# Performance work log

Measured on AMD Instinct MI355X. Metric: run time of the kernel, lower is better.

Reference implementation:

```python
import jax, jax.numpy as jnp
import numpy as np

D = 1024          # d_model
N = 256           # d_state
SQN = 16          # sqrt(d_state), number of blocks / block size
LR = 0.1
BASE_DECAY = 0.05


def setup_inputs() -> dict:
    key = jax.random.key(0)
    ks = jax.random.split(key, 7)
    B, S = 8, 1024
    x = jax.random.normal(ks[0], (B, S, D), dtype=jnp.float32)
    Wk = jax.random.normal(ks[1], (N, D), dtype=jnp.float32) * 0.02
    Wv = jax.random.normal(ks[2], (N, D), dtype=jnp.float32) * 0.02
    Wg = jax.random.normal(ks[3], (1, D), dtype=jnp.float32) * 0.02
    bg = jnp.zeros((1,), dtype=jnp.float32)
    Wo = jax.random.normal(ks[4], (D, N), dtype=jnp.float32) * 0.02
    bo = jnp.zeros((D,), dtype=jnp.float32)
    return {"x": x, "Wk": Wk, "Wv": Wv, "Wg": Wg, "bg": bg, "Wo": Wo, "bo": bo}


def _forward(x, Wk, Wv, Wg, bg, Wo, bo):
    B, S, _ = x.shape
    n = SQN
    dtype = x.dtype
    K = (x @ Wk.T).reshape(B, S, n, n)
    V = (x @ Wv.T).reshape(B, S, n, n)
    gate = jax.nn.sigmoid(x @ Wg.T + bg)  # (B, S, 1)

    w_init = jnp.broadcast_to(jnp.eye(n, dtype=dtype), (n, n, n))       # block identity
    w0 = jnp.broadcast_to(w_init, (B, n, n, n)).astype(dtype)

    def step(carry, inp):
        w1, w2, strength, last_seen, t = carry
        kt, vt, gt = inp  # (B,n,n), (B,n,n), (B,1)
        t = t + 1.0
        # block-diagonal matmuls: hidden[b,i,:] = kt[b,i,:] @ w1[b,i]
        hidden = jnp.einsum('bij,bijk->bik', kt, w1)
        hr = jnp.swapaxes(hidden, -1, -2)  # monarch routing (transpose blocks)
        vt_pred = jnp.einsum('bij,bijk->bik', hr, w2)
        error = vt_pred - vt
        activity = jnp.linalg.norm(kt, axis=-1)  # (B,n)
        delta_t = t - last_seen
        time_gate = 1.0 / jnp.maximum(jnp.log1p(delta_t / 10.0), 1.0)
        decay_rate = BASE_DECAY / (1.0 + strength * time_gate)  # (B,n)
        # TTT gradient step on fast weights
        grad2 = jnp.einsum('bip,biq->bipq', hr, error)
        grad_h = jnp.einsum('bij,bikj->bik', error, w2)
        grad1 = jnp.einsum('bip,biq->bipq', kt, grad_h)
        step_lr = LR * gt[:, :, None, None]  # (B,1,1,1)
        w1 = w1 - step_lr * grad1
        w2 = w2 - step_lr * grad2
        # Ebbinghaus strength / spacing bookkeeping
        err_norm = jnp.linalg.norm(error.reshape(error.shape[0], -1), axis=-1)  # (B,)
        recon_quality = 1.0 / (1.0 + err_norm)
        spacing = jnp.log1p(delta_t) * activity  # (B,n)
        strength = strength + recon_quality[:, None] * spacing * gt * 0.05
        last_seen = jnp.where(activity > 0.1, t, last_seen)
        # decay toward identity init
        df = decay_rate[:, :, None, None]
        w1 = w1 * (1.0 - df) + w_init * df
        w2 = w2 * (1.0 - df) + w_init * df
        yt = jnp.swapaxes(vt_pred, -1, -2).reshape(vt_pred.shape[0], n * n)
        return (w1, w2, strength, last_seen, t), (yt, err_norm)

    carry0 = (w0, w0,
              jnp.zeros((B, n), dtype),
              jnp.zeros((B, n), dtype),
              jnp.asarray(0.0, dtype))
    xs = (jnp.swapaxes(K, 0, 1), jnp.swapaxes(V, 0, 1), jnp.swapaxes(gate, 0, 1))
    _, (ys, errs) = jax.lax.scan(step, carry0, xs)
    output = jnp.swapaxes(ys, 0, 1) @ Wo.T + bo       # (B,S,D)
    error_signal = jnp.swapaxes(errs, 0, 1)[..., None]  # (B,S,1)
    return output, error_signal


def reference(x, Wk, Wv, Wg, bg, Wo, bo):
    return _forward(x, Wk, Wv, Wg, bg, Wo, bo)
```

## Files before the change

kernel.cpp:

```cpp
#include <hip/hip_runtime.h>
#include <hip/hip_bf16.h>

#define B_DIM 8
#define S_DIM 1024
#define D_DIM 1024
#define N_DIM 256
#define M_ROWS (B_DIM * S_DIM)

typedef __attribute__((ext_vector_type(8))) short bf16x8;
typedef __attribute__((ext_vector_type(8))) unsigned short u16x8;
typedef __attribute__((ext_vector_type(4))) float f32x4;
typedef __attribute__((ext_vector_type(2))) float f32x2;

static __device__ __forceinline__ unsigned short f2bf(float f) {
  union { __hip_bfloat16 h; unsigned short s; } u;
  u.h = __float2bfloat16(f);
  return u.s;
}

static __device__ __forceinline__ float log1p_fast(float x) {
  return __logf(1.0f + x);
}

static __device__ __forceinline__ float hsum4(f32x4 v) {
  f32x2 lo = {v[0], v[1]}, hi = {v[2], v[3]};
  f32x2 t = lo + hi;
  return t[0] + t[1];
}

static __device__ __forceinline__ float dpp_swap1(float x) {
  int r = __builtin_amdgcn_update_dpp(0, __builtin_bit_cast(int, x),
                                      0xB1, 0xF, 0xF, true);
  return __builtin_bit_cast(float, r);
}
static __device__ __forceinline__ float pair_sum(float x) {
  return x + dpp_swap1(x);
}

#define LDS_BARRIER()                                         \
  do {                                                        \
    asm volatile("s_waitcnt lgkmcnt(0)" ::: "memory");        \
    __builtin_amdgcn_s_barrier();                             \
    asm volatile("" ::: "memory");                            \
  } while (0)

__global__ __launch_bounds__(256) void gemm_kv(const float* __restrict__ x,
                                               const float* __restrict__ Wk,
                                               const float* __restrict__ Wv,
                                               float* __restrict__ KV) {
  __shared__ unsigned short lsA[128 * 40];
  __shared__ unsigned short lsB[128 * 40];
  const int tid = threadIdx.x;
  const int row0 = blockIdx.y * 128;
  const int col0 = blockIdx.x * 128;
  const float* Bsrc = (col0 < 256) ? (Wk + (size_t)col0 * 1024)
                                   : (Wv + (size_t)(col0 - 256) * 1024);
  const int sr = tid >> 1, sh = tid & 1;
  const float* ap = x + (size_t)(row0 + sr) * 1024 + sh * 16;
  const float* bp = Bsrc + (size_t)sr * 1024 + sh * 16;
  unsigned short* wa = &lsA[sr * 40 + sh * 16];
  unsigned short* wb = &lsB[sr * 40 + sh * 16];

  const int lane = tid & 63;
  const int w = tid >> 6, wr = w >> 1, wc = w & 1;
  const int fr = lane & 15, fk = lane >> 4;

  f32x4 acc[4][4];
#pragma unroll
  for (int m = 0; m < 4; ++m)
#pragma unroll
    for (int n = 0; n < 4; ++n) acc[m][n] = (f32x4){0.f, 0.f, 0.f, 0.f};

  for (int kt = 0; kt < 32; ++kt) {
    const float* a = ap + kt * 32;
    const float* b = bp + kt * 32;
    f32x4 A0 = *(const f32x4*)(a + 0), A1 = *(const f32x4*)(a + 4);
    f32x4 A2 = *(const f32x4*)(a + 8), A3 = *(const f32x4*)(a + 12);
    f32x4 B0 = *(const f32x4*)(b + 0), B1 = *(const f32x4*)(b + 4);
    f32x4 B2 = *(const f32x4*)(b + 8), B3 = *(const f32x4*)(b + 12);
    u16x8 pa0, pa1, pb0, pb1;
#pragma unroll
    for (int e = 0; e < 4; ++e) {
      pa0[e] = f2bf(A0[e]); pa0[e + 4] = f2bf(A1[e]);
      pa1[e] = f2bf(A2[e]); pa1[e + 4] = f2bf(A3[e]);
      pb0[e] = f2bf(B0[e]); pb0[e + 4] = f2bf(B1[e]);
      pb1[e] = f2bf(B2[e]); pb1[e + 4] = f2bf(B3[e]);
    }
    *(u16x8*)wa = pa0; *(u16x8*)(wa + 8) = pa1;
    *(u16x8*)wb = pb0; *(u16x8*)(wb + 8) = pb1;
    __syncthreads();
    bf16x8 af[4], bfr[4];
#pragma unroll
    for (int m = 0; m < 4; ++m)
      af[m] = *(const bf16x8*)(&lsA[(wr * 64 + m * 16 + fr) * 40 + fk * 8]);
#pragma unroll
    for (int n = 0; n < 4; ++n)
      bfr[n] = *(const bf16x8*)(&lsB[(wc * 64 + n * 16 + fr) * 40 + fk * 8]);
#pragma unroll
    for (int m = 0; m < 4; ++m)
#pragma unroll
      for (int n = 0; n < 4; ++n)
        acc[m][n] = __builtin_amdgcn_mfma_f32_16x16x32_bf16(af[m], bfr[n],
                                                            acc[m][n], 0, 0, 0);
    __syncthreads();
  }
#pragma unroll
  for (int m = 0; m < 4; ++m)
#pragma unroll
    for (int n = 0; n < 4; ++n) {
      const int col = col0 + wc * 64 + n * 16 + fr;
#pragma unroll
      for (int r = 0; r < 4; ++r) {
        const int row = row0 + wr * 64 + m * 16 + fk * 4 + r;
        KV[(size_t)row * 512 + col] = acc[m][n][r];
      }
    }
}

__global__ __launch_bounds__(256) void gate_kernel(const float* __restrict__ x,
                                                   const float* __restrict__ Wg,
                                                   const float* __restrict__ bg,
                                                   float* __restrict__ gate) {
  const int row = blockIdx.x * 4 + (threadIdx.x >> 6);
  const int lane = threadIdx.x & 63;
  const f32x4* xr = (const f32x4*)(x + (size_t)row * 1024);
  const f32x4* wg = (const f32x4*)Wg;
  float s = 0.f;
#pragma unroll
  for (int c = 0; c < 4; ++c) {
    f32x4 a = xr[lane + 64 * c];
    f32x4 wv = wg[lane + 64 * c];
    s += a[0] * wv[0] + a[1] * wv[1] + a[2] * wv[2] + a[3] * wv[3];
  }
#pragma unroll
  for (int off = 32; off >= 1; off >>= 1) s += __shfl_xor(s, off, 64);
  if (lane == 0) gate[row] = 1.f / (1.f + __expf(-(s + bg[0])));
}

__global__ __launch_bounds__(256) void wo_perm(const float* __restrict__ Wo,
                                               float* __restrict__ WoP) {
  const int d = blockIdx.x;
  const int c = threadIdx.x;
  WoP[(size_t)d * 256 + c] = Wo[(size_t)d * 256 + ((c & 15) * 16 + (c >> 4))];
}

__global__ __launch_bounds__(256) void act_kernel(const float* __restrict__ KV,
                                                  float* __restrict__ actv) {
  const int idx = blockIdx.x * 256 + threadIdx.x;
  const int bs = idx >> 4, i = idx & 15;
  const f32x4* p = (const f32x4*)(KV + (size_t)bs * 512 + i * 16);
  f32x4 a0 = p[0], a1 = p[1], a2 = p[2], a3 = p[3];
  f32x4 s = a0 * a0 + a1 * a1 + a2 * a2 + a3 * a3;
  actv[idx] = sqrtf(hsum4(s));
}

__global__ __launch_bounds__(512) void scan_kernel(const float* __restrict__ KV,
                                                   const float* __restrict__ gate,
                                                   const float* __restrict__ actv,
                                                   unsigned short* __restrict__ ysbf,
                                                   float* __restrict__ err_out) {
  const int b = blockIdx.x;
  const int tid = threadIdx.x;
  const int i = tid >> 5;
  const int k = (tid >> 1) & 15;
  const int h = tid & 1;
  const int j0 = h * 8;

  __shared__ __align__(16) float hidT[2][16 * 20 + 4];
  __shared__ __align__(16) float errS[256];
  __shared__ __align__(16) float red[2][8];

  if (tid < 16) ((float*)red)[tid] = 0.f;

  f32x4 w1q[2], w2q[2], w2tq[2], eyeq[2];
#pragma unroll
  for (int r = 0; r < 2; ++r) {
    f32x4 v;
#pragma unroll
    for (int e = 0; e < 4; ++e) v[e] = ((j0 + 4 * r + e) == k) ? 1.f : 0.f;
    w1q[r] = v; w2q[r] = v; w2tq[r] = v; eyeq[r] = v;
  }
  float strength = 0.f, last_seen = 0.f, pend = 0.f;

  const float* Kb = KV + (size_t)b * S_DIM * 512;
  const float* Gb = gate + (size_t)b * S_DIM;
  const float* Ab = actv + (size_t)b * S_DIM * 16;
  float* Eb = err_out + (size_t)b * S_DIM;

  const int offK = i * 16 + j0;
  const int offV = 256 + i * 16 + k;

  f32x4 kqA0, kqA1, kqB0, kqB1;
  float vtA, vtB, gA, gB, aA, aB;
  {
    kqA0 = *(const f32x4*)(Kb + offK);
    kqA1 = *(const f32x4*)(Kb + offK + 4);
    vtA = Kb[offV]; gA = Gb[0]; aA = Ab[i];
    kqB0 = *(const f32x4*)(Kb + 512 + offK);
    kqB1 = *(const f32x4*)(Kb + 512 + offK + 4);
    vtB = Kb[512 + offV]; gB = Gb[1]; aB = Ab[16 + i];
  }

  const float* pPre = Kb + 1024;
  const float* pG = Gb + 2;
  const float* pA = Ab + 32 + i;
  unsigned short* pY = ysbf + (size_t)b * S_DIM * 256 + i * 16 + k;

  auto step = [&](int s, f32x4& kq0, f32x4& kq1, float& vt, float& gv,
                  float& av) {
    const int pb = s & 1;
    const float t = (float)(s + 1);

    f32x4 hacc = kq0 * w1q[0] + kq1 * w1q[1];
    const float hidden = pair_sum(hsum4(hacc));
    hidT[pb][k * 20 + i] = hidden;

    const float delta = t - last_seen;
    const float m_pre = fmaxf(log1p_fast(delta * 0.1f), 1.f);
    const float pend_new = log1p_fast(delta) * av * gv * 0.05f;
    const bool seen = (av > 0.1f);

    LDS_BARRIER();

    const f32x4 hq0 = *(const f32x4*)&hidT[pb][i * 20 + j0];
    const f32x4 hq1 = *(const f32x4*)&hidT[pb][i * 20 + j0 + 4];
    const float hkk = hidT[pb][i * 20 + k];

    {
      const f32x4* rp = (const f32x4*)&red[1 - pb][0];
      const f32x4 rs = rp[0] + rp[1];
      const float en = sqrtf(hsum4(rs));
      strength += pend * __builtin_amdgcn_rcpf(1.f + en);
      if (tid == 0 && s != 0) Eb[s - 1] = en;
    }
    const float df = 0.05f * m_pre * __builtin_amdgcn_rcpf(m_pre + strength);
    const float am = 1.f - df;

    f32x4 vacc = hq0 * w2q[0] + hq1 * w2q[1];
    const float vt_pred = pair_sum(hsum4(vacc));
    *pY = f2bf(vt_pred);

    const float err = vt_pred - vt;

    errS[i * 16 + k] = err;
    asm volatile("s_waitcnt lgkmcnt(0)" ::: "memory");
    const f32x4 eq0 = *(const f32x4*)&errS[i * 16 + j0];
    const f32x4 eq1 = *(const f32x4*)&errS[i * 16 + j0 + 4];

    const f32x4 eacc = eq0 * eq0 + eq1 * eq1;
    const float e2row = pair_sum(hsum4(eacc));
    const float e2pair = e2row + __shfl_xor(e2row, 32, 64);
    if ((tid & 63) == 0) red[pb][tid >> 6] = e2pair;

    const f32x4 gacc = eq0 * w2tq[0] + eq1 * w2tq[1];
    const float gh = pair_sum(hsum4(gacc));

    const float slr = 0.1f * gv;
    const float nsga = -slr * gh * am;
    const float nsea = -slr * err * am;
    const float nsha = -slr * hkk * am;
#pragma unroll
    for (int r = 0; r < 2; ++r) {
      const f32x4 kr = (r == 0) ? kq0 : kq1;
      const f32x4 hr = (r == 0) ? hq0 : hq1;
      const f32x4 er = (r == 0) ? eq0 : eq1;
      const f32x4 dfr = eyeq[r] * df;
      w1q[r] = w1q[r] * am + (kr * nsga + dfr);
      w2q[r] = w2q[r] * am + (hr * nsea + dfr);
      w2tq[r] = w2tq[r] * am + (er * nsha + dfr);
    }

    pend = pend_new;
    if (seen) last_seen = t;

    kq0 = *(const f32x4*)(pPre + offK);
    kq1 = *(const f32x4*)(pPre + offK + 4);
    vt = pPre[offV];
    gv = *pG;
    av = *pA;
    pPre += 512; pG += 1; pA += 16; pY += 256;
  };

  for (int s = 0; s < S_DIM; s += 2) {
    step(s, kqA0, kqA1, vtA, gA, aA);
    step(s + 1, kqB0, kqB1, vtB, gB, aB);
  }
  LDS_BARRIER();
  if (tid == 0) {
    const f32x4* rp = (const f32x4*)&red[1][0];
    const f32x4 rs = rp[0] + rp[1];
    Eb[S_DIM - 1] = sqrtf(hsum4(rs));
  }
}

__global__ __launch_bounds__(256) void gemm_out(const unsigned short* __restrict__ ysbf,
                                                const float* __restrict__ WoP,
                                                const float* __restrict__ bo,
                                                float* __restrict__ out) {
  __shared__ unsigned short lsA[128 * 40];
  __shared__ unsigned short lsB[128 * 40];
  const int tid = threadIdx.x;
  const int row0 = blockIdx.y * 128;
  const int col0 = blockIdx.x * 128;
  const int sr = tid >> 1, sh = tid & 1;
  const unsigned short* ap = ysbf + (size_t)(row0 + sr) * 256 + sh * 16;
  const float* bp = WoP + (size_t)(col0 + sr) * 256 + sh * 16;
  unsigned short* wa = &lsA[sr * 40 + sh * 16];
  unsigned short* wb = &lsB[sr * 40 + sh * 16];

  const int lane = tid & 63;
  const int w = tid >> 6, wr = w >> 1, wc = w & 1;
  const int fr = lane & 15, fk = lane >> 4;

  f32x4 acc[4][4];
#pragma unroll
  for (int m = 0; m < 4; ++m)
#pragma unroll
    for (int n = 0; n < 4; ++n) acc[m][n] = (f32x4){0.f, 0.f, 0.f, 0.f};

  for (int kt = 0; kt < 8; ++kt) {
    u16x8 pa0 = *(const u16x8*)(ap + kt * 32);
    u16x8 pa1 = *(const u16x8*)(ap + kt * 32 + 8);
    const float* bq = bp + kt * 32;
    f32x4 B0 = *(const f32x4*)(bq + 0), B1 = *(const f32x4*)(bq + 4);
    f32x4 B2 = *(const f32x4*)(bq + 8), B3 = *(const f32x4*)(bq + 12);
    u16x8 pb0, pb1;
#pragma unroll
    for (int e = 0; e < 4; ++e) {
      pb0[e] = f2bf(B0[e]); pb0[e + 4] = f2bf(B1[e]);
      pb1[e] = f2bf(B2[e]); pb1[e + 4] = f2bf(B3[e]);
    }
    *(u16x8*)wa = pa0; *(u16x8*)(wa + 8) = pa1;
    *(u16x8*)wb = pb0; *(u16x8*)(wb + 8) = pb1;
    __syncthreads();
    bf16x8 af[4], bfr[4];
#pragma unroll
    for (int m = 0; m < 4; ++m)
      af[m] = *(const bf16x8*)(&lsA[(wr * 64 + m * 16 + fr) * 40 + fk * 8]);
#pragma unroll
    for (int n = 0; n < 4; ++n)
      bfr[n] = *(const bf16x8*)(&lsB[(wc * 64 + n * 16 + fr) * 40 + fk * 8]);
#pragma unroll
    for (int m = 0; m < 4; ++m)
#pragma unroll
      for (int n = 0; n < 4; ++n)
        acc[m][n] = __builtin_amdgcn_mfma_f32_16x16x32_bf16(af[m], bfr[n],
                                                            acc[m][n], 0, 0, 0);
    __syncthreads();
  }
#pragma unroll
  for (int m = 0; m < 4; ++m)
#pragma unroll
    for (int n = 0; n < 4; ++n) {
      const int col = col0 + wc * 64 + n * 16 + fr;
      const float bias = bo[col];
#pragma unroll
      for (int r = 0; r < 4; ++r) {
        const int row = row0 + wr * 64 + m * 16 + fk * 4 + r;
        out[(size_t)row * 1024 + col] = acc[m][n][r] + bias;
      }
    }
}

extern "C" void kernel_launch(void* const* d_in, const int* in_sizes, int n_in,
                              void* d_out, int out_size, void* d_ws, size_t ws_size,
                              hipStream_t stream) {
  const float* x = (const float*)d_in[0];
  const float* Wk = (const float*)d_in[1];
  const float* Wv = (const float*)d_in[2];
  const float* Wg = (const float*)d_in[3];
  const float* bg = (const float*)d_in[4];
  const float* Wo = (const float*)d_in[5];
  const float* bo = (const float*)d_in[6];

  float* out = (float*)d_out;
  float* err_out = out + (size_t)M_ROWS * 1024;

  char* ws = (char*)d_ws;
  float* KV = (float*)ws;
  float* gate = (float*)(ws + (size_t)M_ROWS * 512 * 4);
  unsigned short* ysbf =
      (unsigned short*)(ws + (size_t)M_ROWS * 512 * 4 + 32768);
  float* actv = (float*)(ws + (size_t)M_ROWS * 512 * 4 + 32768 +
                         (size_t)M_ROWS * 256 * 2);
  float* WoP = (float*)(ws + (size_t)M_ROWS * 512 * 4 + 32768 +
                        (size_t)M_ROWS * 256 * 2 + (size_t)M_ROWS * 16 * 4);

  gemm_kv<<<dim3(4, 64), 256, 0, stream>>>(x, Wk, Wv, KV);
  act_kernel<<<dim3(512), 256, 0, stream>>>(KV, actv);
  gate_kernel<<<dim3(2048), 256, 0, stream>>>(x, Wg, bg, gate);
  wo_perm<<<dim3(1024), 256, 0, stream>>>(Wo, WoP);
  scan_kernel<<<dim3(8), 512, 0, stream>>>(KV, gate, actv, ysbf, err_out);
  gemm_out<<<dim3(8, 64), 256, 0, stream>>>(ysbf, WoP, bo, out);
}
```

Measured before the change: 821.7 us.

## Precompute next-step hidden via algebraic update to shorten scan critical path

The scan step now computes the next timestep's hidden vector from the pre-update w1, using the rank-1 update identity. It combines am*H0 with a precomputed cross term (k_t·k_{t+1} per block) scaled by the gradient coefficient, plus the decay-to-identity term. This removes the w1 dot product and its barrier dependency from the start of each step, so the hidden values are ready in LDS before the next iteration. The cost is an extra precompute kernel output (crossv), extra per-step loads, and slightly different float rounding.

```diff
diff --git a/kernel.cpp b/kernel.cpp
--- a/kernel.cpp
+++ b/kernel.cpp
@@ -144,19 +144,29 @@
   WoP[(size_t)d * 256 + c] = Wo[(size_t)d * 256 + ((c & 15) * 16 + (c >> 4))];
 }
 
-__global__ __launch_bounds__(256) void act_kernel(const float* __restrict__ KV,
-                                                  float* __restrict__ actv) {
+__global__ __launch_bounds__(256) void act_cross_kernel(const float* __restrict__ KV,
+                                                        float* __restrict__ actv,
+                                                        float* __restrict__ crossv) {
   const int idx = blockIdx.x * 256 + threadIdx.x;
   const int bs = idx >> 4, i = idx & 15;
+  const int s = bs & (S_DIM - 1);
   const f32x4* p = (const f32x4*)(KV + (size_t)bs * 512 + i * 16);
   f32x4 a0 = p[0], a1 = p[1], a2 = p[2], a3 = p[3];
-  f32x4 s = a0 * a0 + a1 * a1 + a2 * a2 + a3 * a3;
-  actv[idx] = sqrtf(hsum4(s));
+  f32x4 sq = a0 * a0 + a1 * a1 + a2 * a2 + a3 * a3;
+  actv[idx] = sqrtf(hsum4(sq));
+  float cr = 0.f;
+  if (s < S_DIM - 1) {
+    const f32x4* q = (const f32x4*)(KV + (size_t)(bs + 1) * 512 + i * 16);
+    f32x4 c4 = a0 * q[0] + a1 * q[1] + a2 * q[2] + a3 * q[3];
+    cr = hsum4(c4);
+  }
+  crossv[idx] = cr;
 }
 
 __global__ __launch_bounds__(512) void scan_kernel(const float* __restrict__ KV,
                                                    const float* __restrict__ gate,
                                                    const float* __restrict__ actv,
+                                                   const float* __restrict__ crossv,
                                                    unsigned short* __restrict__ ysbf,
                                                    float* __restrict__ err_out) {
   const int b = blockIdx.x;
@@ -185,35 +195,42 @@
   const float* Kb = KV + (size_t)b * S_DIM * 512;
   const float* Gb = gate + (size_t)b * S_DIM;
   const float* Ab = actv + (size_t)b * S_DIM * 16;
+  const float* Cb = crossv + (size_t)b * S_DIM * 16;
   float* Eb = err_out + (size_t)b * S_DIM;
 
   const int offK = i * 16 + j0;
-  const int offV = 256 + i * 16 + k;
+  const int offKk = i * 16 + k;
+  const int offV = 256 + offKk;
 
   f32x4 kqA0, kqA1, kqB0, kqB1;
-  float vtA, vtB, gA, gB, aA, aB;
+  float vtA, vtB, ktkA, ktkB, gA, gB, aA, aB, crA, crB;
   {
     kqA0 = *(const f32x4*)(Kb + offK);
     kqA1 = *(const f32x4*)(Kb + offK + 4);
-    vtA = Kb[offV]; gA = Gb[0]; aA = Ab[i];
+    vtA = Kb[offV]; ktkA = Kb[offKk];
+    gA = Gb[0]; aA = Ab[i]; crA = Cb[i];
     kqB0 = *(const f32x4*)(Kb + 512 + offK);
     kqB1 = *(const f32x4*)(Kb + 512 + offK + 4);
-    vtB = Kb[512 + offV]; gB = Gb[1]; aB = Ab[16 + i];
-  }
+    vtB = Kb[512 + offV]; ktkB = Kb[512 + offKk];
+    gB = Gb[1]; aB = Ab[16 + i]; crB = Cb[16 + i];
+  }
+
+  hidT[0][k * 20 + i] = ktkA;
 
   const float* pPre = Kb + 1024;
   const float* pG = Gb + 2;
   const float* pA = Ab + 32 + i;
-  unsigned short* pY = ysbf + (size_t)b * S_DIM * 256 + i * 16 + k;
-
-  auto step = [&](int s, f32x4& kq0, f32x4& kq1, float& vt, float& gv,
-                  float& av) {
+  const float* pC = Cb + 32 + i;
+  unsigned short* pY = ysbf + (size_t)b * S_DIM * 256 + offKk;
+
+  auto step = [&](int s, f32x4& kq0, f32x4& kq1, float& vt, float& ktk,
+                  float& gv, float& av, float& cr,
+                  const f32x4& nkq0, const f32x4& nkq1, float nktk) {
     const int pb = s & 1;
     const float t = (float)(s + 1);
 
-    f32x4 hacc = kq0 * w1q[0] + kq1 * w1q[1];
-    const float hidden = pair_sum(hsum4(hacc));
-    hidT[pb][k * 20 + i] = hidden;
+    f32x4 h0acc = nkq0 * w1q[0] + nkq1 * w1q[1];
+    const float H0 = pair_sum(hsum4(h0acc));
 
     const float delta = t - last_seen;
     const float m_pre = fmaxf(log1p_fast(delta * 0.1f), 1.f);
@@ -242,7 +259,7 @@
 
     const float err = vt_pred - vt;
 
-    errS[i * 16 + k] = err;
+    errS[offKk] = err;
     asm volatile("s_waitcnt lgkmcnt(0)" ::: "memory");
     const f32x4 eq0 = *(const f32x4*)&errS[i * 16 + j0];
     const f32x4 eq1 = *(const f32x4*)&errS[i * 16 + j0 + 4];
@@ -259,6 +276,10 @@
     const float nsga = -slr * gh * am;
     const float nsea = -slr * err * am;
     const float nsha = -slr * hkk * am;
+
+    const float hidden_next = fmaf(am, H0, fmaf(nsga, cr, df * nktk));
+    hidT[pb ^ 1][k * 20 + i] = hidden_next;
+
 #pragma unroll
     for (int r = 0; r < 2; ++r) {
       const f32x4 kr = (r == 0) ? kq0 : kq1;
@@ -276,14 +297,16 @@
     kq0 = *(const f32x4*)(pPre + offK);
     kq1 = *(const f32x4*)(pPre + offK + 4);
     vt = pPre[offV];
+    ktk = pPre[offKk];
     gv = *pG;
     av = *pA;
-    pPre += 512; pG += 1; pA += 16; pY += 256;
+    cr = *pC;
+    pPre += 512; pG += 1; pA += 16; pC += 16; pY += 256;
   };
 
   for (int s = 0; s < S_DIM; s += 2) {
-    step(s, kqA0, kqA1, vtA, gA, aA);
-    step(s + 1, kqB0, kqB1, vtB, gB, aB);
+    step(s, kqA0, kqA1, vtA, ktkA, gA, aA, crA, kqB0, kqB1, ktkB);
+    step(s + 1, kqB0, kqB1, vtB, ktkB, gB, aB, crB, kqA0, kqA1, ktkA);
   }
   LDS_BARRIER();
   if (tid == 0) {
@@ -377,19 +400,19 @@
   float* err_out = out + (size_t)M_ROWS * 1024;
 
   char* ws = (char*)d_ws;
-  float* KV = (float*)ws;
-  float* gate = (float*)(ws + (size_t)M_ROWS * 512 * 4);
-  unsigned short* ysbf =
-      (unsigned short*)(ws + (size_t)M_ROWS * 512 * 4 + 32768);
-  float* actv = (float*)(ws + (size_t)M_ROWS * 512 * 4 + 32768 +
-                         (size_t)M_ROWS * 256 * 2);
-  float* WoP = (float*)(ws + (size_t)M_ROWS * 512 * 4 + 32768 +
-                        (size_t)M_ROWS * 256 * 2 + (size_t)M_ROWS * 16 * 4);
+  size_t off = 0;
+  float* KV = (float*)(ws + off);           off += (size_t)M_ROWS * 512 * 4;
+  float* gate = (float*)(ws + off);         off += (size_t)M_ROWS * 4;
+  unsigned short* ysbf = (unsigned short*)(ws + off);
+                                            off += (size_t)M_ROWS * 256 * 2;
+  float* actv = (float*)(ws + off);         off += (size_t)M_ROWS * 16 * 4;
+  float* crossv = (float*)(ws + off);       off += (size_t)M_ROWS * 16 * 4;
+  float* WoP = (float*)(ws + off);          off += (size_t)D_DIM * 256 * 4;
 
   gemm_kv<<<dim3(4, 64), 256, 0, stream>>>(x, Wk, Wv, KV);
-  act_kernel<<<dim3(512), 256, 0, stream>>>(KV, actv);
+  act_cross_kernel<<<dim3(512), 256, 0, stream>>>(KV, actv, crossv);
   gate_kernel<<<dim3(2048), 256, 0, stream>>>(x, Wg, bg, gate);
   wo_perm<<<dim3(1024), 256, 0, stream>>>(Wo, WoP);
-  scan_kernel<<<dim3(8), 512, 0, stream>>>(KV, gate, actv, ysbf, err_out);
+  scan_kernel<<<dim3(8), 512, 0, stream>>>(KV, gate, actv, crossv, ysbf, err_out);
   gemm_out<<<dim3(8, 64), 256, 0, stream>>>(ysbf, WoP, bo, out);
 }
```

After: 870.6 us. 6.0% more time.
